# Kernel optimization log

Measured on AMD Instinct MI355X. Metric: run time of the kernel, lower is better.

## Reference

```python
import jax, jax.numpy as jnp
import numpy as np

T, B, IN, H, OUT = 16384, 1, 32, 512, 1


def setup_inputs() -> dict:
    key = jax.random.key(0)
    ks = jax.random.split(key, 7)
    s = 0.05
    return {
        "input_seq": jax.random.normal(ks[0], (T, B, IN), dtype=jnp.float32),
        "W_ih": jax.random.normal(ks[1], (4 * H, IN), dtype=jnp.float32) * s,
        "W_hh": jax.random.normal(ks[2], (4 * H, H), dtype=jnp.float32) * s,
        "b_ih": jax.random.normal(ks[3], (4 * H,), dtype=jnp.float32) * s,
        "b_hh": jax.random.normal(ks[4], (4 * H,), dtype=jnp.float32) * s,
        "W_lin": jax.random.normal(ks[5], (OUT, H), dtype=jnp.float32) * s,
        "b_lin": jax.random.normal(ks[6], (OUT,), dtype=jnp.float32) * s,
    }


def reference(input_seq, W_ih, W_hh, b_ih, b_hh, W_lin, b_lin):
    # input_seq: [T, 1, IN]; batch=1 as hardcoded by the module's hidden_cell.
    t = input_seq.shape[0]
    x = input_seq.reshape(t, -1)  # [T, IN]
    h_dim = W_hh.shape[1]
    # Precompute input contribution to gates for all timesteps (one big GEMM).
    x_gates = x @ W_ih.T + (b_ih + b_hh)  # [T, 4H]

    def step(carry, xg):
        h, c = carry
        g = xg + W_hh @ h  # [4H]; PyTorch gate order: i, f, g, o
        i = jax.nn.sigmoid(g[:h_dim])
        f = jax.nn.sigmoid(g[h_dim:2 * h_dim])
        gg = jnp.tanh(g[2 * h_dim:3 * h_dim])
        o = jax.nn.sigmoid(g[3 * h_dim:])
        c_new = f * c + i * gg
        h_new = o * jnp.tanh(c_new)
        return (h_new, c_new), h_new

    h0 = jnp.zeros((h_dim,), dtype=input_seq.dtype)
    c0 = jnp.zeros((h_dim,), dtype=input_seq.dtype)
    _, lstm_out = jax.lax.scan(step, (h0, c0), x_gates)  # [T, H]
    predictions = lstm_out @ W_lin.T + b_lin  # [T, OUT]
    return predictions[-1]  # [OUT]
```

## Files before the change

kernel.cpp:

```cpp
#include <hip/hip_runtime.h>
#include <hip/hip_fp16.h>
#include <math.h>


#define T_STEPS 16384
#define IN_DIM  32
#define H_DIM   512
#define SLOTS   32
#define H_SLICE 16
#define KTOT    544
#define CHUNK   136

typedef unsigned int uint32x4 __attribute__((ext_vector_type(4)));

__device__ __forceinline__ float fast_sigmoid(float v) {
  return 1.0f / (1.0f + __expf(-v));
}
__device__ __forceinline__ float fast_tanh(float v) {
  return 2.0f / (1.0f + __expf(-2.0f * v)) - 1.0f;
}

__device__ __forceinline__ void store_pkt(unsigned int* p, unsigned int v) {
  asm volatile("global_store_dword %0, %1, off sc0 sc1"
               :: "v"(p), "v"(v) : "memory");
}
__device__ __forceinline__ uint32x4 load_pkt4(const unsigned int* p) {
  uint32x4 r;
  asm volatile("global_load_dwordx4 %0, %1, off sc0 sc1\n\ts_waitcnt vmcnt(0)"
               : "=&v"(r) : "v"(p) : "memory");
  return r;
}

__launch_bounds__(256, 1)
__global__ void lstm_scan_kernel(
    const float* __restrict__ x,
    const float* __restrict__ Wih,
    const float* __restrict__ Whh,
    const float* __restrict__ bih,
    const float* __restrict__ bhh,
    const float* __restrict__ Wlin,
    const float* __restrict__ blin,
    float* __restrict__ out,
    unsigned int* pub)
{
  const int slot = blockIdx.x;
  const int tid  = threadIdx.x;
  const int w    = tid >> 6;
  const int l    = tid & 63;

  __shared__ __align__(16) float hshm[KTOT];
  __shared__ float red[256];

  const int R = (l >> 4) * H_DIM + slot * H_SLICE + (l & 15);

  float wreg[CHUNK];
  #pragma unroll
  for (int j = 0; j < CHUNK; ++j) {
    const int k = w * CHUNK + j;
    wreg[j] = (k < H_DIM) ? Whh[R * H_DIM + k]
                          : Wih[R * IN_DIM + (k - H_DIM)];
  }
  #pragma unroll
  for (int j = 0; j < CHUNK; ++j)
    asm volatile("v_mov_b32 %0, %0" : "+v"(wreg[j]));

  const float bias = (w == 0) ? (bih[R] + bhh[R]) : 0.0f;

  float c = 0.0f;

  const bool poller = (tid < 128) && ((tid >> 2) != slot);
  if (tid < H_SLICE) hshm[slot * H_SLICE + tid] = 0.0f;

  for (int t = 0; t < T_STEPS; ++t) {
    float xv = (tid < IN_DIM) ? x[t * IN_DIM + tid] : 0.0f;

    if (poller) {
      const unsigned int* p = pub + (t & 1) * H_DIM + tid * 4;
      const unsigned int tg = (unsigned int)t & 0xFFFFu;
      uint32x4 r;
      for (;;) {
        r = load_pkt4(p);
        if ((r.x >> 16) == tg && (r.y >> 16) == tg &&
            (r.z >> 16) == tg && (r.w >> 16) == tg) break;
      }
      float4 hv4;
      hv4.x = __half2float(__ushort_as_half((unsigned short)(r.x & 0xFFFFu)));
      hv4.y = __half2float(__ushort_as_half((unsigned short)(r.y & 0xFFFFu)));
      hv4.z = __half2float(__ushort_as_half((unsigned short)(r.z & 0xFFFFu)));
      hv4.w = __half2float(__ushort_as_half((unsigned short)(r.w & 0xFFFFu)));
      *(float4*)(hshm + tid * 4) = hv4;
    }
    if (tid < IN_DIM) hshm[H_DIM + tid] = xv;
    __syncthreads();

    const float4* hv = (const float4*)(hshm + w * CHUNK);
    float a0 = 0.f, a1 = 0.f, a2 = 0.f, a3 = 0.f;
    #pragma unroll
    for (int q = 0; q < CHUNK / 4; ++q) {
      const float4 h4 = hv[q];
      a0 = fmaf(wreg[4 * q + 0], h4.x, a0);
      a1 = fmaf(wreg[4 * q + 1], h4.y, a1);
      a2 = fmaf(wreg[4 * q + 2], h4.z, a2);
      a3 = fmaf(wreg[4 * q + 3], h4.w, a3);
    }
    red[w * 64 + l] = (a0 + a1) + (a2 + a3);
    __syncthreads();

    if (w == 0) {
      const float g = bias + red[l] + red[64 + l] + red[128 + l] + red[192 + l];
      const float act = (l < 32 || l >= 48) ? fast_sigmoid(g) : fast_tanh(g);
      const int j = l & 15;
      const float ig = __shfl(act, j, 64);
      const float fg = __shfl(act, j + 16, 64);
      const float gt = __shfl(act, j + 32, 64);
      const float og = __shfl(act, j + 48, 64);
      if (l < H_SLICE) {
        c = fg * c + ig * gt;
        const float h = og * fast_tanh(c);
        hshm[slot * H_SLICE + l] = h;
        const unsigned int pkt =
            (((unsigned int)(t + 1) & 0xFFFFu) << 16) |
            (unsigned int)__half_as_ushort(__float2half_rn(h));
        store_pkt(pub + ((t + 1) & 1) * H_DIM + slot * H_SLICE + l, pkt);
      }
    }
  }

  if (slot == 0) {
    if (poller) {
      const unsigned int* p = pub + (T_STEPS & 1) * H_DIM + tid * 4;
      const unsigned int tg = (unsigned int)T_STEPS & 0xFFFFu;
      uint32x4 r;
      for (;;) {
        r = load_pkt4(p);
        if ((r.x >> 16) == tg && (r.y >> 16) == tg &&
            (r.z >> 16) == tg && (r.w >> 16) == tg) break;
      }
      float4 hv4;
      hv4.x = __half2float(__ushort_as_half((unsigned short)(r.x & 0xFFFFu)));
      hv4.y = __half2float(__ushort_as_half((unsigned short)(r.y & 0xFFFFu)));
      hv4.z = __half2float(__ushort_as_half((unsigned short)(r.z & 0xFFFFu)));
      hv4.w = __half2float(__ushort_as_half((unsigned short)(r.w & 0xFFFFu)));
      *(float4*)(hshm + tid * 4) = hv4;
    }
    __syncthreads();
    red[tid] = hshm[2 * tid] * Wlin[2 * tid] +
               hshm[2 * tid + 1] * Wlin[2 * tid + 1];
    __syncthreads();
    if (w == 0) {
      float s = red[l] + red[64 + l] + red[128 + l] + red[192 + l];
      #pragma unroll
      for (int off = 32; off > 0; off >>= 1) s += __shfl_down(s, off, 64);
      if (l == 0) out[0] = s + blin[0];
    }
  }
}

extern "C" void kernel_launch(void* const* d_in, const int* in_sizes, int n_in,
                              void* d_out, int out_size, void* d_ws, size_t ws_size,
                              hipStream_t stream) {
  const float* x    = (const float*)d_in[0];
  const float* Wih  = (const float*)d_in[1];
  const float* Whh  = (const float*)d_in[2];
  const float* bih  = (const float*)d_in[3];
  const float* bhh  = (const float*)d_in[4];
  const float* Wlin = (const float*)d_in[5];
  const float* blin = (const float*)d_in[6];
  float* out = (float*)d_out;

  unsigned int* pub = (unsigned int*)d_ws;

  hipMemsetAsync(d_ws, 0, 4096, stream);
  hipLaunchKernelGGL(lstm_scan_kernel, dim3(SLOTS), dim3(256), 0, stream,
                     x, Wih, Whh, bih, bhh, Wlin, blin, out, pub);
}
```

Before: 28.58 ms.

## Remap gate rows per wave, drop second barrier, race waves to poll peers

Each wave now owns 4 hidden units across all four gates, with the K dimension split over 4 lanes. The dot-product reduction is done with wave shuffles, which removes the shared-memory reduction and the second __syncthreads per step. The h buffer is double-buffered in LDS. All four waves poll peer packets with staggered sleeps, and an LDS flag lets whichever wave sees the data first publish it to the others. The goal is shorter per-step latency on the serial recurrence, at the cost of redundant activation math in every wave and a more intricate polling protocol.

```diff
diff --git a/kernel.cpp b/kernel.cpp
--- a/kernel.cpp
+++ b/kernel.cpp
@@ -9,7 +9,8 @@
 #define SLOTS   32
 #define H_SLICE 16
 #define KTOT    544
-#define CHUNK   136
+#define CH      136
+#define SPIN    16
 
 typedef unsigned int uint32x4 __attribute__((ext_vector_type(4)));
 
@@ -29,6 +30,9 @@
   asm volatile("global_load_dwordx4 %0, %1, off sc0 sc1\n\ts_waitcnt vmcnt(0)"
                : "=&v"(r) : "v"(p) : "memory");
   return r;
+}
+__device__ __forceinline__ float pkt_to_f(unsigned int v) {
+  return __half2float(__ushort_as_half((unsigned short)(v & 0xFFFFu)));
 }
 
 __launch_bounds__(256, 1)
@@ -48,111 +52,156 @@
   const int w    = tid >> 6;
   const int l    = tid & 63;
 
-  __shared__ __align__(16) float hshm[KTOT];
+  const int gate = l >> 4;
+  const int hi   = (l >> 2) & 3;
+  const int kq   = l & 3;
+
+  __shared__ __align__(16) float buf[2][KTOT];
   __shared__ float red[256];
-
-  const int R = (l >> 4) * H_DIM + slot * H_SLICE + (l & 15);
-
-  float wreg[CHUNK];
+  __shared__ volatile int flag;
+
+  const int R = gate * H_DIM + slot * H_SLICE + w * 4 + hi;
+
+  float wreg[CH];
   #pragma unroll
-  for (int j = 0; j < CHUNK; ++j) {
-    const int k = w * CHUNK + j;
+  for (int j = 0; j < CH; ++j) {
+    const int k = kq * CH + j;
     wreg[j] = (k < H_DIM) ? Whh[R * H_DIM + k]
                           : Wih[R * IN_DIM + (k - H_DIM)];
   }
   #pragma unroll
-  for (int j = 0; j < CHUNK; ++j)
+  for (int j = 0; j < CH; ++j)
     asm volatile("v_mov_b32 %0, %0" : "+v"(wreg[j]));
 
-  const float bias = (w == 0) ? (bih[R] + bhh[R]) : 0.0f;
-
+  const float bias = bih[R] + bhh[R];
   float c = 0.0f;
 
-  const bool poller = (tid < 128) && ((tid >> 2) != slot);
-  if (tid < H_SLICE) hshm[slot * H_SLICE + tid] = 0.0f;
+  const bool own_lane = ((l >> 1) == slot);
+  const bool xthr = (tid < IN_DIM);
+
+  if (tid < H_SLICE) buf[0][slot * H_SLICE + tid] = 0.0f;
+  if (tid == 0) flag = -1;
+  __syncthreads();
+
+  uint32x4 pr0 = {0, 0, 0, 0}, pr1 = {0, 0, 0, 0};
 
   for (int t = 0; t < T_STEPS; ++t) {
-    float xv = (tid < IN_DIM) ? x[t * IN_DIM + tid] : 0.0f;
-
-    if (poller) {
-      const unsigned int* p = pub + (t & 1) * H_DIM + tid * 4;
-      const unsigned int tg = (unsigned int)t & 0xFFFFu;
-      uint32x4 r;
+    float xv = xthr ? x[t * IN_DIM + tid] : 0.0f;
+
+    const unsigned int tg = (unsigned int)t & 0xFFFFu;
+    const unsigned int* pp = pub + (t & 1) * H_DIM + l * 8;
+
+    if (flag != t) {
+      if      (w == 1) __builtin_amdgcn_s_sleep(2);
+      else if (w == 2) __builtin_amdgcn_s_sleep(4);
+      else if (w == 3) __builtin_amdgcn_s_sleep(6);
       for (;;) {
-        r = load_pkt4(p);
-        if ((r.x >> 16) == tg && (r.y >> 16) == tg &&
-            (r.z >> 16) == tg && (r.w >> 16) == tg) break;
+        if (flag == t) break;
+        asm volatile("global_load_dwordx4 %0, %2, off sc0 sc1\n\t"
+                     "global_load_dwordx4 %1, %2, off offset:16 sc0 sc1"
+                     : "+v"(pr0), "+v"(pr1) : "v"(pp) : "memory");
+        int fastexit = 0;
+        #pragma unroll 1
+        for (int s2 = 0; s2 < SPIN; ++s2) {
+          if (flag == t) { fastexit = 1; break; }
+        }
+        if (fastexit) break;
+        asm volatile("s_waitcnt vmcnt(0)"
+                     : "+v"(pr0), "+v"(pr1) :: "memory");
+        const bool ok = own_lane ||
+            ((pr0.x >> 16) == tg && (pr0.y >> 16) == tg &&
+             (pr0.z >> 16) == tg && (pr0.w >> 16) == tg &&
+             (pr1.x >> 16) == tg && (pr1.y >> 16) == tg &&
+             (pr1.z >> 16) == tg && (pr1.w >> 16) == tg);
+        if (__all(ok)) {
+          if (!own_lane) {
+            float4 ha, hb;
+            ha.x = pkt_to_f(pr0.x); ha.y = pkt_to_f(pr0.y);
+            ha.z = pkt_to_f(pr0.z); ha.w = pkt_to_f(pr0.w);
+            hb.x = pkt_to_f(pr1.x); hb.y = pkt_to_f(pr1.y);
+            hb.z = pkt_to_f(pr1.z); hb.w = pkt_to_f(pr1.w);
+            *(float4*)(&buf[t & 1][l * 8])     = ha;
+            *(float4*)(&buf[t & 1][l * 8 + 4]) = hb;
+          }
+          if (l == 0) flag = t;
+          break;
+        }
       }
-      float4 hv4;
-      hv4.x = __half2float(__ushort_as_half((unsigned short)(r.x & 0xFFFFu)));
-      hv4.y = __half2float(__ushort_as_half((unsigned short)(r.y & 0xFFFFu)));
-      hv4.z = __half2float(__ushort_as_half((unsigned short)(r.z & 0xFFFFu)));
-      hv4.w = __half2float(__ushort_as_half((unsigned short)(r.w & 0xFFFFu)));
-      *(float4*)(hshm + tid * 4) = hv4;
-    }
-    if (tid < IN_DIM) hshm[H_DIM + tid] = xv;
+    }
+    if (xthr) buf[t & 1][H_DIM + tid] = xv;
     __syncthreads();
 
-    const float4* hv = (const float4*)(hshm + w * CHUNK);
+    const float4* hv = (const float4*)(&buf[t & 1][kq * CH]);
     float a0 = 0.f, a1 = 0.f, a2 = 0.f, a3 = 0.f;
     #pragma unroll
-    for (int q = 0; q < CHUNK / 4; ++q) {
+    for (int q = 0; q < CH / 4; ++q) {
       const float4 h4 = hv[q];
       a0 = fmaf(wreg[4 * q + 0], h4.x, a0);
       a1 = fmaf(wreg[4 * q + 1], h4.y, a1);
       a2 = fmaf(wreg[4 * q + 2], h4.z, a2);
       a3 = fmaf(wreg[4 * q + 3], h4.w, a3);
     }
-    red[w * 64 + l] = (a0 + a1) + (a2 + a3);
-    __syncthreads();
-
-    if (w == 0) {
-      const float g = bias + red[l] + red[64 + l] + red[128 + l] + red[192 + l];
-      const float act = (l < 32 || l >= 48) ? fast_sigmoid(g) : fast_tanh(g);
-      const int j = l & 15;
-      const float ig = __shfl(act, j, 64);
-      const float fg = __shfl(act, j + 16, 64);
-      const float gt = __shfl(act, j + 32, 64);
-      const float og = __shfl(act, j + 48, 64);
-      if (l < H_SLICE) {
-        c = fg * c + ig * gt;
-        const float h = og * fast_tanh(c);
-        hshm[slot * H_SLICE + l] = h;
-        const unsigned int pkt =
-            (((unsigned int)(t + 1) & 0xFFFFu) << 16) |
-            (unsigned int)__half_as_ushort(__float2half_rn(h));
-        store_pkt(pub + ((t + 1) & 1) * H_DIM + slot * H_SLICE + l, pkt);
+    float s = (a0 + a1) + (a2 + a3);
+    s += __shfl_xor(s, 1, 64);
+    s += __shfl_xor(s, 2, 64);
+    const float g = s + bias;
+    const float act = (gate == 2) ? fast_tanh(g) : fast_sigmoid(g);
+
+    const int base = l & 15;
+    const float ig = __shfl(act, base,      64);
+    const float fg = __shfl(act, base + 16, 64);
+    const float gt = __shfl(act, base + 32, 64);
+    const float og = __shfl(act, base + 48, 64);
+    c = fg * c + ig * gt;
+    const float h = og * fast_tanh(c);
+
+    asm volatile("s_waitcnt vmcnt(0)" : "+v"(pr0), "+v"(pr1) :: "memory");
+
+    if (gate == 0 && kq == 0) {
+      const int hidx = slot * H_SLICE + w * 4 + hi;
+      buf[(t + 1) & 1][hidx] = h;
+      const unsigned int pkt =
+          (((unsigned int)(t + 1) & 0xFFFFu) << 16) |
+          (unsigned int)__half_as_ushort(__float2half_rn(h));
+      store_pkt(pub + ((t + 1) & 1) * H_DIM + hidx, pkt);
+    }
+  }
+
+  asm volatile("s_waitcnt vmcnt(0)" : "+v"(pr0), "+v"(pr1) :: "memory");
+
+  if (slot != 0) return;
+  if (w == 0) {
+    const unsigned int* p = pub + l * 8;
+    const unsigned int tg = (unsigned int)T_STEPS & 0xFFFFu;
+    if (l >= 2) {
+      for (;;) {
+        uint32x4 r0 = load_pkt4(p);
+        uint32x4 r1 = load_pkt4(p + 4);
+        if ((r0.x >> 16) == tg && (r0.y >> 16) == tg &&
+            (r0.z >> 16) == tg && (r0.w >> 16) == tg &&
+            (r1.x >> 16) == tg && (r1.y >> 16) == tg &&
+            (r1.z >> 16) == tg && (r1.w >> 16) == tg) {
+          float4 ha, hb;
+          ha.x = pkt_to_f(r0.x); ha.y = pkt_to_f(r0.y);
+          ha.z = pkt_to_f(r0.z); ha.w = pkt_to_f(r0.w);
+          hb.x = pkt_to_f(r1.x); hb.y = pkt_to_f(r1.y);
+          hb.z = pkt_to_f(r1.z); hb.w = pkt_to_f(r1.w);
+          *(float4*)(&buf[0][l * 8])     = ha;
+          *(float4*)(&buf[0][l * 8 + 4]) = hb;
+          break;
+        }
       }
     }
   }
-
-  if (slot == 0) {
-    if (poller) {
-      const unsigned int* p = pub + (T_STEPS & 1) * H_DIM + tid * 4;
-      const unsigned int tg = (unsigned int)T_STEPS & 0xFFFFu;
-      uint32x4 r;
-      for (;;) {
-        r = load_pkt4(p);
-        if ((r.x >> 16) == tg && (r.y >> 16) == tg &&
-            (r.z >> 16) == tg && (r.w >> 16) == tg) break;
-      }
-      float4 hv4;
-      hv4.x = __half2float(__ushort_as_half((unsigned short)(r.x & 0xFFFFu)));
-      hv4.y = __half2float(__ushort_as_half((unsigned short)(r.y & 0xFFFFu)));
-      hv4.z = __half2float(__ushort_as_half((unsigned short)(r.z & 0xFFFFu)));
-      hv4.w = __half2float(__ushort_as_half((unsigned short)(r.w & 0xFFFFu)));
-      *(float4*)(hshm + tid * 4) = hv4;
-    }
-    __syncthreads();
-    red[tid] = hshm[2 * tid] * Wlin[2 * tid] +
-               hshm[2 * tid + 1] * Wlin[2 * tid + 1];
-    __syncthreads();
-    if (w == 0) {
-      float s = red[l] + red[64 + l] + red[128 + l] + red[192 + l];
-      #pragma unroll
-      for (int off = 32; off > 0; off >>= 1) s += __shfl_down(s, off, 64);
-      if (l == 0) out[0] = s + blin[0];
-    }
+  __syncthreads();
+  red[tid] = buf[0][2 * tid] * Wlin[2 * tid] +
+             buf[0][2 * tid + 1] * Wlin[2 * tid + 1];
+  __syncthreads();
+  if (w == 0) {
+    float s2 = red[l] + red[64 + l] + red[128 + l] + red[192 + l];
+    #pragma unroll
+    for (int off = 32; off > 0; off >>= 1) s2 += __shfl_down(s2, off, 64);
+    if (l == 0) out[0] = s2 + blin[0];
   }
 }
 
```

Result: slower. 68.44 ms (+139.5%).
